# Performance work log

Measured on AMD Instinct MI355X. Metric: run time of the kernel, lower is better.

## Reference

```python
import jax, jax.numpy as jnp
import numpy as np

D = 128          # kg_emb_dim
H = 8            # mha_n_heads
N = 20000        # sub-graph nodes per modality
NNZ = 500000     # incidence entries per modality
E = 5000         # hyperedges per modality
C = 50           # context entities
NENT = 50000     # n_entity (rec vocab)


def hyperconv(x, theta, bias, nodes, edges, num_edges):
    # PyG-style HypergraphConv: out = D^-1 H B^-1 H^T (X Theta) + b
    xt = x @ theta                                             # [N, D]
    ones = jnp.ones(nodes.shape[0], xt.dtype)
    e_sum = jax.ops.segment_sum(xt[nodes], edges, num_segments=num_edges)   # [E, D]
    e_deg = jax.ops.segment_sum(ones, edges, num_segments=num_edges)        # [E]
    m = e_sum / jnp.maximum(e_deg, 1.0)[:, None]               # hyperedge means
    n_sum = jax.ops.segment_sum(m[edges], nodes, num_segments=x.shape[0])   # [N, D]
    n_deg = jax.ops.segment_sum(ones, nodes, num_segments=x.shape[0])       # [N]
    return n_sum / jnp.maximum(n_deg, 1.0)[:, None] + bias


def mha(q_x, kv_x, Wq, bq, Wk, bk, Wv, bv, Wo, bo):
    # torch.nn.MultiheadAttention math, batch of 1 (squeezed)
    dh = D // H
    q = (q_x @ Wq + bq).reshape(-1, H, dh)
    k = (kv_x @ Wk + bk).reshape(-1, H, dh)
    v = (kv_x @ Wv + bv).reshape(-1, H, dh)
    scores = jnp.einsum('qhd,khd->hqk', q, k) / jnp.sqrt(jnp.asarray(dh, q.dtype))
    attn = jax.nn.softmax(scores, axis=-1)
    out = jnp.einsum('hqk,khd->qhd', attn, v).reshape(-1, D)
    return out @ Wo + bo


def self_attn(h, a, b):
    # SelfAttentionBatch: softmax(tanh(h a) b) weighted sum over rows
    e = (jnp.tanh(h @ a) @ b)[:, 0]
    return jax.nn.softmax(e) @ h


def setup_inputs() -> dict:
    ks = jax.random.split(jax.random.key(0), 32)
    s = D ** (-0.5)
    inp = {
        'item_emb':   jax.random.normal(ks[0], (N, D), jnp.float32) * s,
        'entity_emb': jax.random.normal(ks[1], (N, D), jnp.float32) * s,
        'word_emb':   jax.random.normal(ks[2], (N, D), jnp.float32) * s,
        'context_entity': jax.random.normal(ks[3], (C, D), jnp.float32) * s,
        'theta_item':   jax.random.normal(ks[4], (D, D), jnp.float32) * s,
        'bias_item':    jax.random.normal(ks[5], (D,), jnp.float32) * 0.02,
        'theta_entity': jax.random.normal(ks[6], (D, D), jnp.float32) * s,
        'bias_entity':  jax.random.normal(ks[7], (D,), jnp.float32) * 0.02,
        'theta_word':   jax.random.normal(ks[8], (D, D), jnp.float32) * s,
        'bias_word':    jax.random.normal(ks[9], (D,), jnp.float32) * 0.02,
        'Wq': jax.random.normal(ks[10], (D, D), jnp.float32) * s,
        'bq': jax.random.normal(ks[11], (D,), jnp.float32) * 0.02,
        'Wk': jax.random.normal(ks[12], (D, D), jnp.float32) * s,
        'bk': jax.random.normal(ks[13], (D,), jnp.float32) * 0.02,
        'Wv': jax.random.normal(ks[14], (D, D), jnp.float32) * s,
        'bv': jax.random.normal(ks[15], (D,), jnp.float32) * 0.02,
        'Wo': jax.random.normal(ks[16], (D, D), jnp.float32) * s,
        'bo': jax.random.normal(ks[17], (D,), jnp.float32) * 0.02,
        'a_his': jax.random.normal(ks[18], (D, D), jnp.float32) * s,
        'b_his': jax.random.normal(ks[19], (D, 1), jnp.float32) * s,
        'a_kg':  jax.random.normal(ks[20], (D, D), jnp.float32) * s,
        'b_kg':  jax.random.normal(ks[21], (D, 1), jnp.float32) * s,
        'rec_W': jax.random.normal(ks[22], (D, NENT), jnp.float32) * s,
        'rec_b': jax.random.normal(ks[23], (NENT,), jnp.float32) * 0.02,
        'item_nodes':   jax.random.randint(ks[24], (NNZ,), 0, N, jnp.int32),
        'item_edges':   jax.random.randint(ks[25], (NNZ,), 0, E, jnp.int32),
        'entity_nodes': jax.random.randint(ks[26], (NNZ,), 0, N, jnp.int32),
        'entity_edges': jax.random.randint(ks[27], (NNZ,), 0, E, jnp.int32),
        'word_nodes':   jax.random.randint(ks[28], (NNZ,), 0, N, jnp.int32),
        'word_edges':   jax.random.randint(ks[29], (NNZ,), 0, E, jnp.int32),
    }
    return inp


def reference(item_emb, entity_emb, word_emb, context_entity,
              theta_item, bias_item, theta_entity, bias_entity, theta_word, bias_word,
              Wq, bq, Wk, bk, Wv, bv, Wo, bo,
              a_his, b_his, a_kg, b_kg, rec_W, rec_b,
              item_nodes, item_edges, entity_nodes, entity_edges, word_nodes, word_edges):
    ih = hyperconv(item_emb, theta_item, bias_item, item_nodes, item_edges, E)
    eh = hyperconv(entity_emb, theta_entity, bias_entity, entity_nodes, entity_edges, E)
    wh = hyperconv(word_emb, theta_word, bias_word, word_nodes, word_edges, E)
    related = jnp.concatenate([ih, eh, wh], axis=0)            # [3N, D]
    # MHItemAttention: context queries attend over related embeddings
    attentive = mha(context_entity, related, Wq, bq, Wk, bk, Wv, bv, Wo, bo)  # [C, D]
    u = self_attn(attentive, a_his, b_his)                     # [D]
    user = jnp.concatenate([context_entity, u[None]], axis=0)  # [C+1, D]
    user_repr = self_attn(user, a_kg, b_kg)                    # [D]
    scores = user_repr @ rec_W + rec_b                         # [NENT]
    return scores
```

## Files before the change

kernel.cpp:

```cpp
#include <hip/hip_runtime.h>
#include <hip/hip_bf16.h>

#define D_ 128
#define H_ 8
#define N_ 20000
#define NNZ_ 500000
#define E_ 5000
#define C_ 50
#define NENT_ 50000
#define NK_ (3*N_)
#define CAPE_ 192
#define CAPN_ 64
#define ENT_PB 4096
#define NBKT 157
#define BCAP 3648
#define ABLK 123
#define NCH3 118
#define KVBLK 235

struct Ptr3f { const float* p[3]; };
struct Ptr3i { const int* p[3]; };
struct GemmB { const float* A[3]; const float* W[3]; unsigned short* C[3]; };

typedef short bf16x8 __attribute__((ext_vector_type(8)));
typedef float f32x4  __attribute__((ext_vector_type(4)));
typedef float f32x2  __attribute__((ext_vector_type(2)));

__device__ __forceinline__ unsigned short f2b(float f){
  unsigned u = __float_as_uint(f);
  u += 0x7FFFu + ((u>>16)&1u);
  return (unsigned short)(u>>16);
}
__device__ __forceinline__ unsigned pk2(float a, float b){
  return (unsigned)f2b(a) | ((unsigned)f2b(b) << 16);
}
__device__ __forceinline__ float blo(unsigned u){ return __uint_as_float(u<<16); }
__device__ __forceinline__ float bhi(unsigned u){ return __uint_as_float(u & 0xFFFF0000u); }

#define GBATCH(SRC, SREG, LBASE) { \
  uint4 uu[8]; \
  _Pragma("unroll") \
  for (int kk=0;kk<8;kk++){ \
    int idx = __shfl(SREG, (LBASE) + 4*kk + rgrp); \
    uu[kk] = *(const uint4*)((SRC) + (size_t)idx*128 + dl*8); \
  } \
  _Pragma("unroll") \
  for (int kk=0;kk<8;kk++){ \
    a01 += (f32x2){blo(uu[kk].x), bhi(uu[kk].x)}; \
    a23 += (f32x2){blo(uu[kk].y), bhi(uu[kk].y)}; \
    a45 += (f32x2){blo(uu[kk].z), bhi(uu[kk].z)}; \
    a67 += (f32x2){blo(uu[kk].w), bhi(uu[kk].w)}; \
  } }

#define PB_PACK 7500
#define PB_Z    7628
#define PB_Q    7629
#define PB_CTX  7693
#define PB_TOT  7743
__global__ __launch_bounds__(256) void prep(Ptr3f xs, unsigned short* __restrict__ xb,
    const float* __restrict__ Wk, const float* __restrict__ Wv, unsigned short* __restrict__ bfB,
    int* __restrict__ gcnt_e, int* __restrict__ gcnt_n, unsigned short* __restrict__ mzero,
    const float* __restrict__ ctx, const float* __restrict__ Wq, const float* __restrict__ bq,
    unsigned short* __restrict__ bfQ,
    const float* __restrict__ a2, const float* __restrict__ b2, float* __restrict__ e2)
{
  int bid = blockIdx.x, t = threadIdx.x;
  if (bid < PB_PACK){
    int mod = bid / 2500, blk = bid - mod*2500;
    int i4 = blk*256 + t;
    float4 v = *(const float4*)(xs.p[mod] + (size_t)i4*4);
    ushort4 o; o.x=f2b(v.x); o.y=f2b(v.y); o.z=f2b(v.z); o.w=f2b(v.w);
    *(ushort4*)(xb + (size_t)mod*N_*D_ + (size_t)i4*4) = o;
  } else if (bid < PB_Z){
    int idx = (bid - PB_PACK)*256 + t;
    int j  = idx & 7;
    int L  = (idx >> 3) & 63;
    int kb = (idx >> 9) & 3;
    int tt = idx >> 11;
    int k = kb*32 + (L>>4)*8 + j;
    int x = L & 15;
    float v = (tt < 8) ? Wk[(size_t)k*128 + tt*16 + x] : Wv[(size_t)k*128 + (tt-8)*16 + x];
    bfB[idx] = f2b(v);
  } else if (bid == PB_Z){
    for (int i=t; i<3*NBKT; i+=256){ gcnt_e[i]=0; gcnt_n[i]=0; }
    if (t < 64)       ((unsigned*)(xb    + (size_t)60000*128))[t]    = 0u;
    else if (t < 128) ((unsigned*)(mzero + (size_t)15000*128))[t-64] = 0u;
  } else if (bid < PB_CTX){
    int idx = (bid - PB_Q)*256 + t;
    int j  = idx & 7;
    int L  = (idx >> 3) & 63;
    int qt = (idx >> 9) & 3;
    int h  = idx >> 11;
    int k  = ((L>>4)&3)*8 + j;
    int q  = qt*16 + (L & 15);
    float val = 0.f;
    if (k < 16 && q < C_){
      const float* cr = ctx + (size_t)q*128;
      const float* wc = Wq + h*16 + k;
      float s0=0.f,s1=0.f,s2=0.f,s3=0.f;
      for (int d=0; d<128; d+=4){
        s0 = fmaf(cr[d],   wc[(size_t) d   *128], s0);
        s1 = fmaf(cr[d+1], wc[(size_t)(d+1)*128], s1);
        s2 = fmaf(cr[d+2], wc[(size_t)(d+2)*128], s2);
        s3 = fmaf(cr[d+3], wc[(size_t)(d+3)*128], s3);
      }
      val = 0.25f * (s0+s1+s2+s3 + bq[h*16+k]);
    }
    bfQ[idx] = f2b(val);
  } else {
    __shared__ float row[128];
    __shared__ float ps[128][2];
    __shared__ float red[2];
    int q = bid - PB_CTX;
    if (t < 128) row[t] = ctx[(size_t)q*128 + t];
    __syncthreads();
    int c = t & 127, half = t >> 7;
    float s = 0.f;
    int d0 = half*64;
    for (int d=d0; d<d0+64; d+=4){
      s = fmaf(row[d],   a2[(size_t) d   *128 + c], s);
      s = fmaf(row[d+1], a2[(size_t)(d+1)*128 + c], s);
      s = fmaf(row[d+2], a2[(size_t)(d+2)*128 + c], s);
      s = fmaf(row[d+3], a2[(size_t)(d+3)*128 + c], s);
    }
    ps[c][half] = s;
    __syncthreads();
    if (t < 128){
      float v = tanhf(ps[t][0] + ps[t][1]) * b2[t];
      #pragma unroll
      for (int k=32; k>=1; k>>=1) v += __shfl_xor(v, k);
      if ((t & 63) == 0) red[t>>6] = v;
    }
    __syncthreads();
    if (t == 0) e2[q] = red[0] + red[1];
  }
}

__global__ __launch_bounds__(256) void binA(Ptr3i nodes, Ptr3i edges,
    unsigned* __restrict__ pe_part, unsigned* __restrict__ pn_part,
    int* __restrict__ gcnt_e, int* __restrict__ gcnt_n)
{
  __shared__ unsigned lbin[ENT_PB];
  __shared__ int cnt[256], off[256];
  __shared__ int gbase[NBKT];
  __shared__ int wsum[4];
  const int mod = blockIdx.y;
  const int* nd = nodes.p[mod];
  const int* ed = edges.p[mod];
  const int base = blockIdx.x * ENT_PB;
  const int t = threadIdx.x;
  const int lane = t & 63, w = t >> 6;

  int myn[16], mye[16], pos[16];
  #pragma unroll
  for (int k=0;k<16;k++){
    int i = base + t + k*256;
    if (i < NNZ_){ myn[k]=nd[i]; mye[k]=ed[i]; }
    else { myn[k]=-1; mye[k]=-1; }
  }

  cnt[t] = 0;
  __syncthreads();
  #pragma unroll
  for (int k=0;k<16;k++)
    if (mye[k] >= 0) pos[k] = atomicAdd(&cnt[mye[k]>>5], 1);
  __syncthreads();
  {
    int v = cnt[t], s = v;
    #pragma unroll
    for (int d=1; d<64; d<<=1){ int u=__shfl_up(s,d); if (lane>=d) s+=u; }
    if (lane==63) wsum[w]=s;
    __syncthreads();
    int wb=0;
    for (int i=0;i<w;i++) wb+=wsum[i];
    off[t] = wb + s - v;
    __syncthreads();
  }
  #pragma unroll
  for (int k=0;k<16;k++)
    if (mye[k] >= 0)
      lbin[off[mye[k]>>5] + pos[k]] = ((unsigned)mye[k] << 15) | (unsigned)myn[k];
  if (t < NBKT && cnt[t] > 0) gbase[t] = atomicAdd(&gcnt_e[mod*NBKT + t], cnt[t]);
  __syncthreads();
  {
    int total = off[255];
    unsigned* dstreg = pe_part + (size_t)mod*NBKT*BCAP;
    for (int i=t; i<total; i+=256){
      unsigned pk = lbin[i];
      int b = pk >> 20;
      int gp = gbase[b] + (i - off[b]);
      if (gp < BCAP) dstreg[(size_t)b*BCAP + gp] = pk;
    }
  }
  __syncthreads();

  cnt[t] = 0;
  __syncthreads();
  #pragma unroll
  for (int k=0;k<16;k++)
    if (myn[k] >= 0) pos[k] = atomicAdd(&cnt[myn[k]>>7], 1);
  __syncthreads();
  {
    int v = cnt[t], s = v;
    #pragma unroll
    for (int d=1; d<64; d<<=1){ int u=__shfl_up(s,d); if (lane>=d) s+=u; }
    if (lane==63) wsum[w]=s;
    __syncthreads();
    int wb=0;
    for (int i=0;i<w;i++) wb+=wsum[i];
    off[t] = wb + s - v;
    __syncthreads();
  }
  #pragma unroll
  for (int k=0;k<16;k++)
    if (myn[k] >= 0)
      lbin[off[myn[k]>>7] + pos[k]] = ((unsigned)myn[k] << 13) | (unsigned)mye[k];
  if (t < NBKT && cnt[t] > 0) gbase[t] = atomicAdd(&gcnt_n[mod*NBKT + t], cnt[t]);
  __syncthreads();
  {
    int total = off[255];
    unsigned* dstreg = pn_part + (size_t)mod*NBKT*BCAP;
    for (int i=t; i<total; i+=256){
      unsigned pk = lbin[i];
      int b = pk >> 20;
      int gp = gbase[b] + (i - off[b]);
      if (gp < BCAP) dstreg[(size_t)b*BCAP + gp] = pk;
    }
  }
}

__global__ __launch_bounds__(256) void binB(const unsigned* __restrict__ pe_part,
    const unsigned* __restrict__ pn_part,
    const int* __restrict__ gcnt_e, const int* __restrict__ gcnt_n,
    int* __restrict__ cnt_all,
    unsigned short* __restrict__ e_slot, unsigned short* __restrict__ n_slot)
{
  __shared__ unsigned short ls[128*CAPN_];
  __shared__ int lc[128];
  const int y = blockIdx.y, b = blockIdx.x, t = threadIdx.x;
  if (y < 3){
    const int mod = y;
    {
      unsigned short dmy = (unsigned short)(60000 - mod*20000);
      unsigned dd = (unsigned)dmy * 0x10001u;
      unsigned* lsu32 = (unsigned*)ls;
      for (int i=t; i<32*CAPE_/2; i+=256) lsu32[i] = dd;
    }
    if (t < 32) lc[t] = 0;
    __syncthreads();
    int cnt = gcnt_e[mod*NBKT + b];
    if (cnt > BCAP) cnt = BCAP;
    const unsigned* src = pe_part + ((size_t)mod*NBKT + b)*BCAP;
    for (int i=t; i<cnt; i+=256){
      unsigned pk = src[i];
      int el = (pk >> 15) - b*32;
      int n  = pk & 0x7FFF;
      int p = atomicAdd(&lc[el], 1);
      if (p < CAPE_) ls[el*CAPE_ + p] = (unsigned short)n;
    }
    __syncthreads();
    int rows = E_ - b*32; if (rows > 32) rows = 32;
    if (t < rows) cnt_all[mod*(E_+N_) + b*32 + t] = lc[t];
    const unsigned* lsu = (const unsigned*)ls;
    unsigned* dst = (unsigned*)(e_slot + ((size_t)mod*E_ + b*32)*CAPE_);
    int tot = rows*CAPE_/2;
    for (int i=t; i<tot; i+=256) dst[i] = lsu[i];
  } else {
    const int mod = y - 3;
    {
      unsigned short dmy = (unsigned short)(15000 - mod*5000);
      unsigned dd = (unsigned)dmy * 0x10001u;
      unsigned* lsu32 = (unsigned*)ls;
      for (int i=t; i<128*CAPN_/2; i+=256) lsu32[i] = dd;
    }
    if (t < 128) lc[t] = 0;
    __syncthreads();
    int cnt = gcnt_n[mod*NBKT + b];
    if (cnt > BCAP) cnt = BCAP;
    const unsigned* src = pn_part + ((size_t)mod*NBKT + b)*BCAP;
    for (int i=t; i<cnt; i+=256){
      unsigned pk = src[i];
      int nl = (pk >> 13) - b*128;
      int e  = pk & 0x1FFF;
      int p = atomicAdd(&lc[nl], 1);
      if (p < CAPN_) ls[nl*CAPN_ + p] = (unsigned short)e;
    }
    __syncthreads();
    int rows = N_ - b*128; if (rows > 128) rows = 128;
    if (t < rows) cnt_all[mod*(E_+N_) + E_ + b*128 + t] = lc[t];
    const unsigned* lsu = (const unsigned*)ls;
    unsigned* dst = (unsigned*)(n_slot + ((size_t)mod*N_ + b*128)*CAPN_);
    int tot = rows*CAPN_/2;
    for (int i=t; i<tot; i+=256) dst[i] = lsu[i];
  }
}

#define EGB 3752
__global__ __launch_bounds__(256) void e_gather_w(const unsigned short* __restrict__ xb,
    const int* __restrict__ cnt_all, const unsigned short* __restrict__ e_slot,
    float* __restrict__ m_mean)
{
  const int bid = blockIdx.x;
  const int x = bid & 7, k = bid >> 3;
  int mod, r;
  if (x < 6){
    mod = x / 3;
    int li = x - mod*3;
    int c = 417 - (li == 2);
    if (k < c){
      r = k*3 + li;
    } else {
      int hg = 52*x + (x >= 3) + (k - c);
      mod = 2; r = 938 + hg;
      if (r >= E_/4) return;
    }
  } else {
    mod = 2; r = k*2 + (x - 6);
  }
  const int w = threadIdx.x >> 6, lane = threadIdx.x & 63;
  const int rgrp = lane >> 4, dl = lane & 15;
  const int e = r*4 + w;
  const unsigned short* xt = xb + (size_t)mod*N_*D_;
  int cnt = cnt_all[mod*(E_+N_) + e];
  int c2 = (cnt < CAPE_) ? cnt : CAPE_;
  int c2p = (c2 + 31) & ~31;
  const unsigned short* slot = e_slot + ((size_t)mod*E_ + e)*CAPE_;
  int sv0 = slot[lane], sv1 = slot[64 + lane], sv2 = slot[128 + lane];
  f32x2 a01={0.f,0.f}, a23={0.f,0.f}, a45={0.f,0.f}, a67={0.f,0.f};

  if (c2p > 0)   GBATCH(xt, sv0, 0);
  if (c2p > 32)  GBATCH(xt, sv0, 32);
  if (c2p > 64)  GBATCH(xt, sv1, 0);
  if (c2p > 96)  GBATCH(xt, sv1, 32);
  if (c2p > 128) GBATCH(xt, sv2, 0);
  if (c2p > 160) GBATCH(xt, sv2, 32);

  float a0=a01.x, a1=a01.y, a2=a23.x, a3=a23.y, a4=a45.x, a5=a45.y, a6=a67.x, a7=a67.y;
  #pragma unroll
  for (int s=16; s<=32; s<<=1){
    a0 += __shfl_xor(a0, s); a1 += __shfl_xor(a1, s);
    a2 += __shfl_xor(a2, s); a3 += __shfl_xor(a3, s);
    a4 += __shfl_xor(a4, s); a5 += __shfl_xor(a5, s);
    a6 += __shfl_xor(a6, s); a7 += __shfl_xor(a7, s);
  }
  if (rgrp == 0){
    float inv = 1.f / fmaxf((float)cnt, 1.f);
    float* dst = m_mean + ((size_t)mod*E_ + e)*128 + dl*8;
    float4 o1; o1.x=a0*inv; o1.y=a1*inv; o1.z=a2*inv; o1.w=a3*inv;
    float4 o2; o2.x=a4*inv; o2.y=a5*inv; o2.z=a6*inv; o2.w=a7*inv;
    *(float4*)dst = o1;
    *(float4*)(dst + 4) = o2;
  }
}

__global__ __launch_bounds__(256) void gemm_b(GemmB g, int M)
{
  const float* A = g.A[blockIdx.y];
  const float* W = g.W[blockIdx.y];
  unsigned short* Cout = g.C[blockIdx.y];
  __shared__ float As[64][33];
  __shared__ float Ws[32][128];
  const int t  = threadIdx.x;
  const int br = blockIdx.x * 64;
  const int r0 = (t >> 5) * 8;
  const int c0 = (t & 31) * 4;
  const int lr = t >> 2;
  const int lk = (t & 3) * 8;
  const int wk = t >> 5;

  float acc[8][4];
  #pragma unroll
  for (int i=0;i<8;i++){ acc[i][0]=0.f; acc[i][1]=0.f; acc[i][2]=0.f; acc[i][3]=0.f; }

  for (int kb=0; kb<128; kb+=32){
    float av[8];
    const int grow = br + lr;
    if (grow < M){
      const float* p = A + (size_t)grow*128 + kb + lk;
      float4 a = ((const float4*)p)[0], b = ((const float4*)p)[1];
      av[0]=a.x;av[1]=a.y;av[2]=a.z;av[3]=a.w;av[4]=b.x;av[5]=b.y;av[6]=b.z;av[7]=b.w;
    } else {
      #pragma unroll
      for (int j=0;j<8;j++) av[j]=0.f;
    }
    float4 wv4[4];
    #pragma unroll
    for (int kk=0;kk<4;kk++) wv4[kk] = *(const float4*)&W[(size_t)(kb + wk + kk*8)*128 + c0];

    __syncthreads();
    #pragma unroll
    for (int j=0;j<8;j++) As[lr][lk+j] = av[j];
    #pragma unroll
    for (int kk=0;kk<4;kk++) *(float4*)&Ws[wk + kk*8][c0] = wv4[kk];
    __syncthreads();

    #pragma unroll
    for (int k=0;k<32;k++){
      float4 wv = *(const float4*)&Ws[k][c0];
      #pragma unroll
      for (int i=0;i<8;i++){
        float a = As[r0+i][k];
        acc[i][0] = fmaf(a, wv.x, acc[i][0]);
        acc[i][1] = fmaf(a, wv.y, acc[i][1]);
        acc[i][2] = fmaf(a, wv.z, acc[i][2]);
        acc[i][3] = fmaf(a, wv.w, acc[i][3]);
      }
    }
  }

  #pragma unroll
  for (int i=0;i<8;i++){
    int gr = br + r0 + i;
    if (gr < M){
      ushort4 o;
      o.x=f2b(acc[i][0]); o.y=f2b(acc[i][1]); o.z=f2b(acc[i][2]); o.w=f2b(acc[i][3]);
      *(ushort4*)(Cout + (size_t)gr*128 + c0) = o;
    }
  }
}

__global__ __launch_bounds__(256) void n_gather_w(const unsigned short* __restrict__ m_buf,
    const int* __restrict__ cnt_all, const unsigned short* __restrict__ n_slot,
    Ptr3f biases, unsigned short* __restrict__ relbf)
{
  int mod = blockIdx.y;
  int w = threadIdx.x >> 6, lane = threadIdx.x & 63;
  int rgrp = lane >> 4, dl = lane & 15;
  int n = blockIdx.x*4 + w;
  const unsigned short* m = m_buf + (size_t)mod*E_*D_;
  int cnt = cnt_all[mod*(E_+N_) + E_ + n];
  int c2 = (cnt < CAPN_) ? cnt : CAPN_;
  int c2p = (c2 + 31) & ~31;
  const unsigned short* slot = n_slot + ((size_t)mod*N_ + n)*CAPN_;
  int sv = slot[lane];
  f32x2 a01={0.f,0.f}, a23={0.f,0.f}, a45={0.f,0.f}, a67={0.f,0.f};
  if (c2p > 0)  GBATCH(m, sv, 0);
  if (c2p > 32) GBATCH(m, sv, 32);

  float a0=a01.x, a1=a01.y, a2=a23.x, a3=a23.y, a4=a45.x, a5=a45.y, a6=a67.x, a7=a67.y;
  #pragma unroll
  for (int s=16; s<=32; s<<=1){
    a0 += __shfl_xor(a0, s); a1 += __shfl_xor(a1, s);
    a2 += __shfl_xor(a2, s); a3 += __shfl_xor(a3, s);
    a4 += __shfl_xor(a4, s); a5 += __shfl_xor(a5, s);
    a6 += __shfl_xor(a6, s); a7 += __shfl_xor(a7, s);
  }
  if (rgrp == 0){
    float inv = 1.f / fmaxf((float)cnt, 1.f);
    const float* bs = biases.p[mod] + dl*8;
    uint4 o;
    o.x = pk2(a0*inv + bs[0], a1*inv + bs[1]);
    o.y = pk2(a2*inv + bs[2], a3*inv + bs[3]);
    o.z = pk2(a4*inv + bs[4], a5*inv + bs[5]);
    o.w = pk2(a6*inv + bs[6], a7*inv + bs[7]);
    *(uint4*)(relbf + ((size_t)mod*N_ + n)*128 + dl*8) = o;
  }
}

__global__ __launch_bounds__(256) void gemm_kv_mfma(const unsigned short* __restrict__ relbf,
    const unsigned short* __restrict__ bfB, const float* __restrict__ bk,
    const float* __restrict__ bv, unsigned short* __restrict__ Kb,
    unsigned short* __restrict__ Vtg)
{
  __shared__ unsigned short Bs[32768];
  const int t = threadIdx.x, w = t >> 6, L = t & 63;
  const int m = L & 15, quad = L >> 4, x = m;

  {
    const uint4* src = (const uint4*)bfB;
    uint4* dst = (uint4*)Bs;
    for (int i = t; i < 4096; i += 256) dst[i] = src[i];
  }
  __syncthreads();

  const int rowbase = blockIdx.x*256;
  for (int g = 0; g < 4; g++){
    const int j0 = rowbase + g*64 + w*16;

    bf16x8 a[4];
    {
      int row = j0 + m;
      int rowc = (row < NK_) ? row : (NK_-1);
      #pragma unroll
      for (int kb=0; kb<4; kb++)
        a[kb] = *(const bf16x8*)(relbf + (size_t)rowc*128 + kb*32 + quad*8);
    }

    f32x4 acc[16];
    #pragma unroll
    for (int tt=0; tt<16; tt++) acc[tt] = (f32x4){0.f,0.f,0.f,0.f};

    #pragma unroll
    for (int kb=0; kb<4; kb++){
      #pragma unroll
      for (int tt=0; tt<16; tt++){
        bf16x8 b = *(const bf16x8*)&Bs[(((tt*4 + kb)*64 + L) << 3)];
        acc[tt] = __builtin_amdgcn_mfma_f32_16x16x32_bf16(a[kb], b, acc[tt], 0, 0, 0);
      }
    }

    #pragma unroll
    for (int tt=0; tt<16; tt++){
      int h = tt & 7, kv = tt >> 3;
      float bias = (kv ? bv : bk)[h*16 + x];
      #pragma unroll
      for (int r=0; r<4; r++){
        int jr = j0 + quad*4 + r;
        if (jr < NK_){
          unsigned short val = f2b(acc[tt][r] + bias);
          if (kv == 0) Kb[(((size_t)h*NK_ + jr) << 4) + x] = val;
          else         Vtg[((size_t)(h*16 + x))*NK_ + jr] = val;
        }
      }
    }
  }
}

__global__ __launch_bounds__(256) void flash3(const unsigned short* __restrict__ Kb,
    const unsigned short* __restrict__ Vtg, const unsigned short* __restrict__ bfQ,
    float* __restrict__ part)
{
  __shared__ unsigned short P_lds[4][64][40];
  __shared__ float mbuf[4][64][18];
  const int c = blockIdx.x, h = blockIdx.y;
  const int t = threadIdx.x, w = t >> 6, L = t & 63;
  const int n = L & 15, quad = L >> 4;

  bf16x8 qb[4];
  #pragma unroll
  for (int qt=0; qt<4; qt++)
    qb[qt] = *(const bf16x8*)(bfQ + (((h*4 + qt)*64 + L) << 3));

  float Mc[4], Lc[4];
  f32x4 accq[4];
  #pragma unroll
  for (int qt=0; qt<4; qt++){ Mc[qt] = -INFINITY; Lc[qt] = 0.f; accq[qt] = (f32x4){0.f,0.f,0.f,0.f}; }

  const int base = c*512 + w*128;
  unsigned* Pw = (unsigned*)&P_lds[w][0][0];

  for (int tile=0; tile<4; tile++){
    const int j0 = base + tile*32;
    const bool dead = (j0 >= NK_);

    bf16x8 a0 = (bf16x8){0,0,0,0,0,0,0,0};
    bf16x8 a1 = a0;
    if (quad < 2){
      int k0 = j0 + n;      if (k0 > NK_-1) k0 = NK_-1;
      int k1 = j0 + 16 + n; if (k1 > NK_-1) k1 = NK_-1;
      a0 = *(const bf16x8*)(Kb + (((size_t)h*NK_ + k0) << 4) + quad*8);
      a1 = *(const bf16x8*)(Kb + (((size_t)h*NK_ + k1) << 4) + quad*8);
    }
    f32x4 s0[4], s1[4];
    #pragma unroll
    for (int qt=0; qt<4; qt++){
      s0[qt] = __builtin_amdgcn_mfma_f32_16x16x32_bf16(a0, qb[qt], (f32x4){0.f,0.f,0.f,0.f}, 0,0,0);
      s1[qt] = __builtin_amdgcn_mfma_f32_16x16x32_bf16(a1, qb[qt], (f32x4){0.f,0.f,0.f,0.f}, 0,0,0);
    }

    #pragma unroll
    for (int qt=0; qt<4; qt++){
      float mt = s0[qt][0];
      mt = fmaxf(mt, s0[qt][1]); mt = fmaxf(mt, s0[qt][2]); mt = fmaxf(mt, s0[qt][3]);
      mt = fmaxf(mt, s1[qt][0]); mt = fmaxf(mt, s1[qt][1]);
      mt = fmaxf(mt, s1[qt][2]); mt = fmaxf(mt, s1[qt][3]);
      mt = fmaxf(mt, __shfl_xor(mt, 16));
      mt = fmaxf(mt, __shfl_xor(mt, 32));
      float Mn = fmaxf(Mc[qt], mt);
      float corr = __expf(Mc[qt] - Mn);
      Mc[qt] = Mn;
      float p0[4], p1[4];
      #pragma unroll
      for (int r=0;r<4;r++){
        p0[r] = __expf(s0[qt][r] - Mn);
        p1[r] = __expf(s1[qt][r] - Mn);
      }
      if (dead){
        #pragma unroll
        for (int r=0;r<4;r++){ p0[r]=0.f; p1[r]=0.f; }
      }
      float lt = p0[0]+p0[1]+p0[2]+p0[3]+p1[0]+p1[1]+p1[2]+p1[3];
      lt += __shfl_xor(lt, 16);
      lt += __shfl_xor(lt, 32);
      Lc[qt] = Lc[qt]*corr + lt;
      int rb = (qt*16 + n)*20;
      Pw[rb + quad*2]     = pk2(p0[0], p0[1]);
      Pw[rb + quad*2 + 1] = pk2(p0[2], p0[3]);
      Pw[rb + 8 + quad*2]     = pk2(p1[0], p1[1]);
      Pw[rb + 8 + quad*2 + 1] = pk2(p1[2], p1[3]);
      #pragma unroll
      for (int r=0;r<4;r++){
        float cr = __shfl(corr, quad*4 + r);
        accq[qt][r] *= cr;
      }
    }
    __syncthreads();

    bf16x8 bv_;
    {
      int va = j0 + quad*8; if (va > NK_-8) va = NK_-8;
      bv_ = *(const bf16x8*)(Vtg + ((size_t)(h*16 + n))*NK_ + va);
    }
    #pragma unroll
    for (int qt=0; qt<4; qt++){
      bf16x8 pa = *(const bf16x8*)&P_lds[w][qt*16 + n][quad*8];
      accq[qt] = __builtin_amdgcn_mfma_f32_16x16x32_bf16(pa, bv_, accq[qt], 0,0,0);
    }
    __syncthreads();
  }

  #pragma unroll
  for (int qt=0; qt<4; qt++){
    #pragma unroll
    for (int r=0; r<4; r++)
      mbuf[w][qt*16 + quad*4 + r][2 + n] = accq[qt][r];
    if (quad == 0){
      mbuf[w][qt*16 + n][0] = Mc[qt];
      mbuf[w][qt*16 + n][1] = Lc[qt];
    }
  }
  __syncthreads();
  if (t < C_){
    float M = mbuf[0][t][0], Lm = mbuf[0][t][1];
    float A[16];
    #pragma unroll
    for (int i=0;i<16;i++) A[i] = mbuf[0][t][2+i];
    #pragma unroll
    for (int ww=1; ww<4; ww++){
      float pm = mbuf[ww][t][0], pl = mbuf[ww][t][1];
      if (pl > 0.f){
        float mn = fmaxf(M, pm);
        float c1 = __expf(M - mn), c2 = __expf(pm - mn);
        Lm = Lm*c1 + pl*c2;
        #pragma unroll
        for (int i=0;i<16;i++) A[i] = A[i]*c1 + mbuf[ww][t][2+i]*c2;
        M = mn;
      }
    }
    float* pp = part + ((size_t)(h*NCH3 + c)*C_ + t)*18;
    pp[0] = M; pp[1] = Lm;
    #pragma unroll
    for (int i=0;i<16;i++) pp[2+i] = A[i];
  }
}

__global__ __launch_bounds__(512) void merge_oproj_e1(const float* __restrict__ part,
    const float* __restrict__ Wo, const float* __restrict__ bo,
    const float* __restrict__ a1, const float* __restrict__ b1,
    float* __restrict__ attentive, float* __restrict__ e1)
{
  __shared__ float row[128];
  __shared__ float ps[128][4];
  __shared__ float orow[128];
  __shared__ float red[2];
  const int q = blockIdx.x, t = threadIdx.x;
  const int h = t >> 6, lane = t & 63;

  {
    float M = -1e30f, L = 0.f;
    float A[16];
    #pragma unroll
    for (int i=0;i<16;i++) A[i] = 0.f;

    #pragma unroll
    for (int cc=0; cc<2; cc++){
      int c = lane + cc*64;
      if (c < NCH3){
        const float* p = part + ((size_t)(h*NCH3 + c)*C_ + q)*18;
        float pm = p[0], pl = p[1];
        if (pl > 0.f){
          float Mn = fmaxf(M, pm);
          float w1 = __expf(M - Mn), w2 = __expf(pm - Mn);
          L = L*w1 + pl*w2;
          #pragma unroll
          for (int i=0;i<16;i++) A[i] = fmaf(A[i], w1, p[2+i]*w2);
          M = Mn;
        }
      }
    }
    #pragma unroll
    for (int d=32; d>=1; d>>=1){
      float pm = __shfl_xor(M, d);
      float pl = __shfl_xor(L, d);
      float Ao[16];
      #pragma unroll
      for (int i=0;i<16;i++) Ao[i] = __shfl_xor(A[i], d);
      float Mn = fmaxf(M, pm);
      float w1 = __expf(M - Mn), w2 = __expf(pm - Mn);
      L = L*w1 + pl*w2;
      #pragma unroll
      for (int i=0;i<16;i++) A[i] = fmaf(A[i], w1, Ao[i]*w2);
      M = Mn;
    }
    if (lane == 0){
      float invL = 1.f / L;
      #pragma unroll
      for (int i=0;i<16;i++) row[h*16 + i] = A[i]*invL;
    }
  }
  __syncthreads();

  const int c = t & 127, seg = t >> 7;
  {
    float s = 0.f;
    int d0 = seg*32;
    for (int d=d0; d<d0+32; d+=4){
      s = fmaf(row[d],   Wo[(size_t) d   *128 + c], s);
      s = fmaf(row[d+1], Wo[(size_t)(d+1)*128 + c], s);
      s = fmaf(row[d+2], Wo[(size_t)(d+2)*128 + c], s);
      s = fmaf(row[d+3], Wo[(size_t)(d+3)*128 + c], s);
    }
    ps[c][seg] = s;
  }
  __syncthreads();
  if (t < 128){
    float o = ps[t][0]+ps[t][1]+ps[t][2]+ps[t][3] + bo[t];
    attentive[(size_t)q*128 + t] = o;
    orow[t] = o;
  }
  __syncthreads();
  {
    float s = 0.f;
    int d0 = seg*32;
    for (int d=d0; d<d0+32; d+=4){
      s = fmaf(orow[d],   a1[(size_t) d   *128 + c], s);
      s = fmaf(orow[d+1], a1[(size_t)(d+1)*128 + c], s);
      s = fmaf(orow[d+2], a1[(size_t)(d+2)*128 + c], s);
      s = fmaf(orow[d+3], a1[(size_t)(d+3)*128 + c], s);
    }
    ps[c][seg] = s;
  }
  __syncthreads();
  if (t < 128){
    float v = tanhf(ps[t][0]+ps[t][1]+ps[t][2]+ps[t][3]) * b1[t];
    #pragma unroll
    for (int k=32; k>=1; k>>=1) v += __shfl_xor(v, k);
    if ((t & 63) == 0) red[t>>6] = v;
  }
  __syncthreads();
  if (t == 0) e1[q] = red[0] + red[1];
}

__global__ __launch_bounds__(256) void tail_scores(const float* __restrict__ attentive,
    const float* __restrict__ ctx, const float* __restrict__ a2, const float* __restrict__ b2,
    const float* __restrict__ e1, const float* __restrict__ e2,
    const float* __restrict__ recW, const float* __restrict__ recb, float* __restrict__ out)
{
  __shared__ float p[64];
  __shared__ float u[128];
  __shared__ float red[2];
  __shared__ float p2[64];
  __shared__ float ur[128];
  const int t = threadIdx.x;

  if (t == 0){
    float mx=-INFINITY;
    for (int i=0;i<C_;i++) mx=fmaxf(mx,e1[i]);
    float ss=0.f;
    for (int i=0;i<C_;i++){ p[i]=__expf(e1[i]-mx); ss+=p[i]; }
    float inv=1.f/ss;
    for (int i=0;i<C_;i++) p[i]*=inv;
  }
  __syncthreads();
  if (t < 128){
    float s=0.f;
    for (int r=0;r<C_;r++) s = fmaf(p[r], attentive[(size_t)r*128 + t], s);
    u[t] = s;
  }
  __syncthreads();
  if (t < 128){
    float s0=0.f,s1=0.f,s2=0.f,s3=0.f;
    for (int d=0; d<128; d+=4){
      s0 = fmaf(u[d],   a2[(size_t) d   *128 + t], s0);
      s1 = fmaf(u[d+1], a2[(size_t)(d+1)*128 + t], s1);
      s2 = fmaf(u[d+2], a2[(size_t)(d+2)*128 + t], s2);
      s3 = fmaf(u[d+3], a2[(size_t)(d+3)*128 + t], s3);
    }
    float v = tanhf(s0+s1+s2+s3) * b2[t];
    #pragma unroll
    for (int k=32; k>=1; k>>=1) v += __shfl_xor(v, k);
    if ((t & 63) == 0) red[t>>6] = v;
  }
  __syncthreads();
  if (t == 0){
    float elast = red[0] + red[1];
    float mx=elast;
    for (int i=0;i<C_;i++) mx=fmaxf(mx,e2[i]);
    float ss=0.f;
    for (int i=0;i<C_;i++){ p2[i]=__expf(e2[i]-mx); ss+=p2[i]; }
    float pl = __expf(elast-mx); ss += pl;
    float inv=1.f/ss;
    for (int i=0;i<C_;i++) p2[i]*=inv;
    p2[C_] = pl*inv;
  }
  __syncthreads();
  if (t < 128){
    float s=0.f;
    for (int r=0;r<C_;r++) s = fmaf(p2[r], ctx[(size_t)r*128 + t], s);
    s = fmaf(p2[C_], u[t], s);
    ur[t] = s;
  }
  __syncthreads();
  int j = blockIdx.x*256 + t;
  if (j < NENT_){
    float s0=0.f,s1=0.f,s2=0.f,s3=0.f;
    for (int d=0; d<128; d+=4){
      s0 = fmaf(ur[d],   recW[(size_t) d   *NENT_ + j], s0);
      s1 = fmaf(ur[d+1], recW[(size_t)(d+1)*NENT_ + j], s1);
      s2 = fmaf(ur[d+2], recW[(size_t)(d+2)*NENT_ + j], s2);
      s3 = fmaf(ur[d+3], recW[(size_t)(d+3)*NENT_ + j], s3);
    }
    out[j] = s0+s1+s2+s3 + recb[j];
  }
}

extern "C" void kernel_launch(void* const* d_in, const int* in_sizes, int n_in,
                              void* d_out, int out_size, void* d_ws, size_t ws_size,
                              hipStream_t stream)
{
  auto f32 = [&](int i){ return (const float*)d_in[i]; };
  Ptr3i nodes = {{(const int*)d_in[24], (const int*)d_in[26], (const int*)d_in[28]}};
  Ptr3i edges = {{(const int*)d_in[25], (const int*)d_in[27], (const int*)d_in[29]}};

  char* base = (char*)d_ws;
  int*   cnt_all = (int*)base;
  int*   gcnt_e  = (int*)(base + 300064);
  int*   gcnt_n  = gcnt_e + NBKT*3;
  unsigned short* n_slot = (unsigned short*)(base + 300064 + 4096);
  float* m_mean  = (float*)((char*)n_slot + 7680000);
  unsigned short* m_buf = (unsigned short*)((char*)m_mean + 7680000);
  unsigned short* relbf = (unsigned short*)((char*)m_buf + 3840256);
  unsigned short* bfB   = (unsigned short*)((char*)relbf + 15360000);
  unsigned short* bfQ   = (unsigned short*)((char*)bfB + 65536);
  float* attentive = (float*)((char*)bfQ + 32768);
  float* user_repr = (float*)((char*)attentive + 25600);
  float* e1buf     = user_repr + 128;
  float* e2buf     = e1buf + 64;
  float* fpart = (float*)relbf;
  char* U = (char*)(e2buf + 64);
  unsigned* pe_part = (unsigned*)U;
  unsigned* pn_part = pe_part + (size_t)3*NBKT*BCAP;
  unsigned short* e_slot = (unsigned short*)(pn_part + (size_t)3*NBKT*BCAP);
  unsigned short* xb     = e_slot + (size_t)3*E_*CAPE_;
  unsigned short* Kb  = (unsigned short*)U;
  unsigned short* Vtg = Kb + (size_t)H_*NK_*16;

  Ptr3f xs = {{f32(0), f32(1), f32(2)}};
  prep<<<PB_TOT, 256, 0, stream>>>(xs, xb, f32(12), f32(14), bfB, gcnt_e, gcnt_n, m_buf,
                                   f32(3), f32(10), f32(11), bfQ, f32(20), f32(21), e2buf);

  binA<<<dim3(ABLK, 3), 256, 0, stream>>>(nodes, edges, pe_part, pn_part, gcnt_e, gcnt_n);
  binB<<<dim3(NBKT, 6), 256, 0, stream>>>(pe_part, pn_part, gcnt_e, gcnt_n, cnt_all,
                                          e_slot, n_slot);

  e_gather_w<<<EGB, 256, 0, stream>>>(xb, cnt_all, e_slot, m_mean);
  GemmB g;
  for (int mod=0; mod<3; mod++){
    g.A[mod] = m_mean + (size_t)mod*E_*D_;
    g.W[mod] = f32(4 + 2*mod);
    g.C[mod] = m_buf + (size_t)mod*E_*D_;
  }
  gemm_b<<<dim3((E_+63)/64, 3), 256, 0, stream>>>(g, E_);
  Ptr3f biases = {{f32(5), f32(7), f32(9)}};
  n_gather_w<<<dim3(N_/4, 3), 256, 0, stream>>>(m_buf, cnt_all, n_slot, biases, relbf);

  gemm_kv_mfma<<<KVBLK, 256, 0, stream>>>(relbf, bfB, f32(13), f32(15), Kb, Vtg);
  flash3<<<dim3(NCH3, H_), 256, 0, stream>>>(Kb, Vtg, bfQ, fpart);
  merge_oproj_e1<<<C_, 512, 0, stream>>>(fpart, f32(16), f32(17), f32(18), f32(19),
                                         attentive, e1buf);

  tail_scores<<<(NENT_+255)/256, 256, 0, stream>>>(attentive, f32(3), f32(20), f32(21),
                                                   e1buf, e2buf, f32(22), f32(23), (float*)d_out);
}
```

Before: 336.2 us.

## Fuse binning kernels into prep and edge-gather launches to overlap independent work

Moves the first binning pass into the prep kernel as extra blocks, and splits the second binning pass so the node-side binning runs in the same launch as the hyperedge gather. Counter zeroing moves to a memset before the launch. The aim is to overlap independent stages and cut launch and tail idle time. The risk is that the fused kernels carry the larger shared-memory footprint for every block, which may reduce occupancy for the lightweight prep blocks.

```diff
diff --git a/kernel.cpp b/kernel.cpp
--- a/kernel.cpp
+++ b/kernel.cpp
@@ -17,6 +17,9 @@
 #define ABLK 123
 #define NCH3 118
 #define KVBLK 235
+#define BINA_B (3*ABLK)
+#define NBB (3*NBKT)
+#define EGB 3752
 
 struct Ptr3f { const float* p[3]; };
 struct Ptr3i { const int* p[3]; };
@@ -57,14 +60,109 @@
 #define PB_Q    7629
 #define PB_CTX  7693
 #define PB_TOT  7743
-__global__ __launch_bounds__(256) void prep(Ptr3f xs, unsigned short* __restrict__ xb,
+__global__ __launch_bounds__(256) void prep_binA(Ptr3f xs, unsigned short* __restrict__ xb,
     const float* __restrict__ Wk, const float* __restrict__ Wv, unsigned short* __restrict__ bfB,
-    int* __restrict__ gcnt_e, int* __restrict__ gcnt_n, unsigned short* __restrict__ mzero,
+    unsigned short* __restrict__ mzero,
     const float* __restrict__ ctx, const float* __restrict__ Wq, const float* __restrict__ bq,
     unsigned short* __restrict__ bfQ,
-    const float* __restrict__ a2, const float* __restrict__ b2, float* __restrict__ e2)
-{
-  int bid = blockIdx.x, t = threadIdx.x;
+    const float* __restrict__ a2, const float* __restrict__ b2, float* __restrict__ e2,
+    Ptr3i nodes, Ptr3i edges,
+    unsigned* __restrict__ pe_part, unsigned* __restrict__ pn_part,
+    int* __restrict__ gcnt_e, int* __restrict__ gcnt_n)
+{
+  const int t = threadIdx.x;
+  if (blockIdx.x < BINA_B){
+    __shared__ unsigned lbin[ENT_PB];
+    __shared__ int cnt[256], off[256];
+    __shared__ int gbase[NBKT];
+    __shared__ int wsum[4];
+    const int mod = blockIdx.x / ABLK;
+    const int xblk = blockIdx.x - mod*ABLK;
+    const int* nd = nodes.p[mod];
+    const int* ed = edges.p[mod];
+    const int base = xblk * ENT_PB;
+    const int lane = t & 63, w = t >> 6;
+
+    int myn[16], mye[16], pos[16];
+    #pragma unroll
+    for (int k=0;k<16;k++){
+      int i = base + t + k*256;
+      if (i < NNZ_){ myn[k]=nd[i]; mye[k]=ed[i]; }
+      else { myn[k]=-1; mye[k]=-1; }
+    }
+
+    cnt[t] = 0;
+    __syncthreads();
+    #pragma unroll
+    for (int k=0;k<16;k++)
+      if (mye[k] >= 0) pos[k] = atomicAdd(&cnt[mye[k]>>5], 1);
+    __syncthreads();
+    {
+      int v = cnt[t], s = v;
+      #pragma unroll
+      for (int d=1; d<64; d<<=1){ int u=__shfl_up(s,d); if (lane>=d) s+=u; }
+      if (lane==63) wsum[w]=s;
+      __syncthreads();
+      int wb=0;
+      for (int i=0;i<w;i++) wb+=wsum[i];
+      off[t] = wb + s - v;
+      __syncthreads();
+    }
+    #pragma unroll
+    for (int k=0;k<16;k++)
+      if (mye[k] >= 0)
+        lbin[off[mye[k]>>5] + pos[k]] = ((unsigned)mye[k] << 15) | (unsigned)myn[k];
+    if (t < NBKT && cnt[t] > 0) gbase[t] = atomicAdd(&gcnt_e[mod*NBKT + t], cnt[t]);
+    __syncthreads();
+    {
+      int total = off[255];
+      unsigned* dstreg = pe_part + (size_t)mod*NBKT*BCAP;
+      for (int i=t; i<total; i+=256){
+        unsigned pk = lbin[i];
+        int b = pk >> 20;
+        int gp = gbase[b] + (i - off[b]);
+        if (gp < BCAP) dstreg[(size_t)b*BCAP + gp] = pk;
+      }
+    }
+    __syncthreads();
+
+    cnt[t] = 0;
+    __syncthreads();
+    #pragma unroll
+    for (int k=0;k<16;k++)
+      if (myn[k] >= 0) pos[k] = atomicAdd(&cnt[myn[k]>>7], 1);
+    __syncthreads();
+    {
+      int v = cnt[t], s = v;
+      #pragma unroll
+      for (int d=1; d<64; d<<=1){ int u=__shfl_up(s,d); if (lane>=d) s+=u; }
+      if (lane==63) wsum[w]=s;
+      __syncthreads();
+      int wb=0;
+      for (int i=0;i<w;i++) wb+=wsum[i];
+      off[t] = wb + s - v;
+      __syncthreads();
+    }
+    #pragma unroll
+    for (int k=0;k<16;k++)
+      if (myn[k] >= 0)
+        lbin[off[myn[k]>>7] + pos[k]] = ((unsigned)myn[k] << 13) | (unsigned)mye[k];
+    if (t < NBKT && cnt[t] > 0) gbase[t] = atomicAdd(&gcnt_n[mod*NBKT + t], cnt[t]);
+    __syncthreads();
+    {
+      int total = off[255];
+      unsigned* dstreg = pn_part + (size_t)mod*NBKT*BCAP;
+      for (int i=t; i<total; i+=256){
+        unsigned pk = lbin[i];
+        int b = pk >> 20;
+        int gp = gbase[b] + (i - off[b]);
+        if (gp < BCAP) dstreg[(size_t)b*BCAP + gp] = pk;
+      }
+    }
+    return;
+  }
+
+  int bid = blockIdx.x - BINA_B;
   if (bid < PB_PACK){
     int mod = bid / 2500, blk = bid - mod*2500;
     int i4 = blk*256 + t;
@@ -82,7 +180,6 @@
     float v = (tt < 8) ? Wk[(size_t)k*128 + tt*16 + x] : Wv[(size_t)k*128 + (tt-8)*16 + x];
     bfB[idx] = f2b(v);
   } else if (bid == PB_Z){
-    for (int i=t; i<3*NBKT; i+=256){ gcnt_e[i]=0; gcnt_n[i]=0; }
     if (t < 64)       ((unsigned*)(xb    + (size_t)60000*128))[t]    = 0u;
     else if (t < 128) ((unsigned*)(mzero + (size_t)15000*128))[t-64] = 0u;
   } else if (bid < PB_CTX){
@@ -136,137 +233,51 @@
   }
 }
 
-__global__ __launch_bounds__(256) void binA(Ptr3i nodes, Ptr3i edges,
-    unsigned* __restrict__ pe_part, unsigned* __restrict__ pn_part,
-    int* __restrict__ gcnt_e, int* __restrict__ gcnt_n)
-{
-  __shared__ unsigned lbin[ENT_PB];
-  __shared__ int cnt[256], off[256];
-  __shared__ int gbase[NBKT];
-  __shared__ int wsum[4];
-  const int mod = blockIdx.y;
-  const int* nd = nodes.p[mod];
-  const int* ed = edges.p[mod];
-  const int base = blockIdx.x * ENT_PB;
-  const int t = threadIdx.x;
-  const int lane = t & 63, w = t >> 6;
-
-  int myn[16], mye[16], pos[16];
-  #pragma unroll
-  for (int k=0;k<16;k++){
-    int i = base + t + k*256;
-    if (i < NNZ_){ myn[k]=nd[i]; mye[k]=ed[i]; }
-    else { myn[k]=-1; mye[k]=-1; }
-  }
-
-  cnt[t] = 0;
-  __syncthreads();
-  #pragma unroll
-  for (int k=0;k<16;k++)
-    if (mye[k] >= 0) pos[k] = atomicAdd(&cnt[mye[k]>>5], 1);
-  __syncthreads();
+__global__ __launch_bounds__(256) void binB_e(const unsigned* __restrict__ pe_part,
+    const int* __restrict__ gcnt_e, int* __restrict__ cnt_all,
+    unsigned short* __restrict__ e_slot)
+{
+  __shared__ unsigned short ls[32*CAPE_];
+  __shared__ int lc[32];
+  const int mod = blockIdx.y, b = blockIdx.x, t = threadIdx.x;
   {
-    int v = cnt[t], s = v;
-    #pragma unroll
-    for (int d=1; d<64; d<<=1){ int u=__shfl_up(s,d); if (lane>=d) s+=u; }
-    if (lane==63) wsum[w]=s;
-    __syncthreads();
-    int wb=0;
-    for (int i=0;i<w;i++) wb+=wsum[i];
-    off[t] = wb + s - v;
-    __syncthreads();
-  }
-  #pragma unroll
-  for (int k=0;k<16;k++)
-    if (mye[k] >= 0)
-      lbin[off[mye[k]>>5] + pos[k]] = ((unsigned)mye[k] << 15) | (unsigned)myn[k];
-  if (t < NBKT && cnt[t] > 0) gbase[t] = atomicAdd(&gcnt_e[mod*NBKT + t], cnt[t]);
-  __syncthreads();
-  {
-    int total = off[255];
-    unsigned* dstreg = pe_part + (size_t)mod*NBKT*BCAP;
-    for (int i=t; i<total; i+=256){
-      unsigned pk = lbin[i];
-      int b = pk >> 20;
-      int gp = gbase[b] + (i - off[b]);
-      if (gp < BCAP) dstreg[(size_t)b*BCAP + gp] = pk;
-    }
-  }
-  __syncthreads();
-
-  cnt[t] = 0;
-  __syncthreads();
-  #pragma unroll
-  for (int k=0;k<16;k++)
-    if (myn[k] >= 0) pos[k] = atomicAdd(&cnt[myn[k]>>7], 1);
-  __syncthreads();
-  {
-    int v = cnt[t], s = v;
-    #pragma unroll
-    for (int d=1; d<64; d<<=1){ int u=__shfl_up(s,d); if (lane>=d) s+=u; }
-    if (lane==63) wsum[w]=s;
-    __syncthreads();
-    int wb=0;
-    for (int i=0;i<w;i++) wb+=wsum[i];
-    off[t] = wb + s - v;
-    __syncthreads();
-  }
-  #pragma unroll
-  for (int k=0;k<16;k++)
-    if (myn[k] >= 0)
-      lbin[off[myn[k]>>7] + pos[k]] = ((unsigned)myn[k] << 13) | (unsigned)mye[k];
-  if (t < NBKT && cnt[t] > 0) gbase[t] = atomicAdd(&gcnt_n[mod*NBKT + t], cnt[t]);
-  __syncthreads();
-  {
-    int total = off[255];
-    unsigned* dstreg = pn_part + (size_t)mod*NBKT*BCAP;
-    for (int i=t; i<total; i+=256){
-      unsigned pk = lbin[i];
-      int b = pk >> 20;
-      int gp = gbase[b] + (i - off[b]);
-      if (gp < BCAP) dstreg[(size_t)b*BCAP + gp] = pk;
-    }
-  }
-}
-
-__global__ __launch_bounds__(256) void binB(const unsigned* __restrict__ pe_part,
-    const unsigned* __restrict__ pn_part,
-    const int* __restrict__ gcnt_e, const int* __restrict__ gcnt_n,
-    int* __restrict__ cnt_all,
-    unsigned short* __restrict__ e_slot, unsigned short* __restrict__ n_slot)
+    unsigned short dmy = (unsigned short)(60000 - mod*20000);
+    unsigned dd = (unsigned)dmy * 0x10001u;
+    unsigned* lsu32 = (unsigned*)ls;
+    for (int i=t; i<32*CAPE_/2; i+=256) lsu32[i] = dd;
+  }
+  if (t < 32) lc[t] = 0;
+  __syncthreads();
+  int cnt = gcnt_e[mod*NBKT + b];
+  if (cnt > BCAP) cnt = BCAP;
+  const unsigned* src = pe_part + ((size_t)mod*NBKT + b)*BCAP;
+  for (int i=t; i<cnt; i+=256){
+    unsigned pk = src[i];
+    int el = (pk >> 15) - b*32;
+    int n  = pk & 0x7FFF;
+    int p = atomicAdd(&lc[el], 1);
+    if (p < CAPE_) ls[el*CAPE_ + p] = (unsigned short)n;
+  }
+  __syncthreads();
+  int rows = E_ - b*32; if (rows > 32) rows = 32;
+  if (t < rows) cnt_all[mod*(E_+N_) + b*32 + t] = lc[t];
+  const unsigned* lsu = (const unsigned*)ls;
+  unsigned* dst = (unsigned*)(e_slot + ((size_t)mod*E_ + b*32)*CAPE_);
+  int tot = rows*CAPE_/2;
+  for (int i=t; i<tot; i+=256) dst[i] = lsu[i];
+}
+
+__global__ __launch_bounds__(256) void egather_binbn(const unsigned short* __restrict__ xb,
+    const int* __restrict__ cnt_all, const unsigned short* __restrict__ e_slot,
+    float* __restrict__ m_mean,
+    const unsigned* __restrict__ pn_part, const int* __restrict__ gcnt_n,
+    int* __restrict__ cnt_all_w, unsigned short* __restrict__ n_slot)
 {
   __shared__ unsigned short ls[128*CAPN_];
   __shared__ int lc[128];
-  const int y = blockIdx.y, b = blockIdx.x, t = threadIdx.x;
-  if (y < 3){
-    const int mod = y;
-    {
-      unsigned short dmy = (unsigned short)(60000 - mod*20000);
-      unsigned dd = (unsigned)dmy * 0x10001u;
-      unsigned* lsu32 = (unsigned*)ls;
-      for (int i=t; i<32*CAPE_/2; i+=256) lsu32[i] = dd;
-    }
-    if (t < 32) lc[t] = 0;
-    __syncthreads();
-    int cnt = gcnt_e[mod*NBKT + b];
-    if (cnt > BCAP) cnt = BCAP;
-    const unsigned* src = pe_part + ((size_t)mod*NBKT + b)*BCAP;
-    for (int i=t; i<cnt; i+=256){
-      unsigned pk = src[i];
-      int el = (pk >> 15) - b*32;
-      int n  = pk & 0x7FFF;
-      int p = atomicAdd(&lc[el], 1);
-      if (p < CAPE_) ls[el*CAPE_ + p] = (unsigned short)n;
-    }
-    __syncthreads();
-    int rows = E_ - b*32; if (rows > 32) rows = 32;
-    if (t < rows) cnt_all[mod*(E_+N_) + b*32 + t] = lc[t];
-    const unsigned* lsu = (const unsigned*)ls;
-    unsigned* dst = (unsigned*)(e_slot + ((size_t)mod*E_ + b*32)*CAPE_);
-    int tot = rows*CAPE_/2;
-    for (int i=t; i<tot; i+=256) dst[i] = lsu[i];
-  } else {
-    const int mod = y - 3;
+  const int t = threadIdx.x;
+  if (blockIdx.x < NBB){
+    const int mod = blockIdx.x / NBKT, b = blockIdx.x - mod*NBKT;
     {
       unsigned short dmy = (unsigned short)(15000 - mod*5000);
       unsigned dd = (unsigned)dmy * 0x10001u;
@@ -287,21 +298,16 @@
     }
     __syncthreads();
     int rows = N_ - b*128; if (rows > 128) rows = 128;
-    if (t < rows) cnt_all[mod*(E_+N_) + E_ + b*128 + t] = lc[t];
+    if (t < rows) cnt_all_w[mod*(E_+N_) + E_ + b*128 + t] = lc[t];
     const unsigned* lsu = (const unsigned*)ls;
     unsigned* dst = (unsigned*)(n_slot + ((size_t)mod*N_ + b*128)*CAPN_);
     int tot = rows*CAPN_/2;
     for (int i=t; i<tot; i+=256) dst[i] = lsu[i];
-  }
-}
-
-#define EGB 3752
-__global__ __launch_bounds__(256) void e_gather_w(const unsigned short* __restrict__ xb,
-    const int* __restrict__ cnt_all, const unsigned short* __restrict__ e_slot,
-    float* __restrict__ m_mean)
-{
-  const int bid = blockIdx.x;
-  const int x = bid & 7, k = bid >> 3;
+    return;
+  }
+
+  const int bb = blockIdx.x - NBB;
+  const int x = bb & 7, k = bb >> 3;
   int mod, r;
   if (x < 6){
     mod = x / 3;
@@ -317,7 +323,7 @@
   } else {
     mod = 2; r = k*2 + (x - 6);
   }
-  const int w = threadIdx.x >> 6, lane = threadIdx.x & 63;
+  const int w = t >> 6, lane = t & 63;
   const int rgrp = lane >> 4, dl = lane & 15;
   const int e = r*4 + w;
   const unsigned short* xt = xb + (size_t)mod*N_*D_;
@@ -845,15 +851,18 @@
   unsigned short* Kb  = (unsigned short*)U;
   unsigned short* Vtg = Kb + (size_t)H_*NK_*16;
 
+  hipMemsetAsync(gcnt_e, 0, 4096, stream);
+
   Ptr3f xs = {{f32(0), f32(1), f32(2)}};
-  prep<<<PB_TOT, 256, 0, stream>>>(xs, xb, f32(12), f32(14), bfB, gcnt_e, gcnt_n, m_buf,
-                                   f32(3), f32(10), f32(11), bfQ, f32(20), f32(21), e2buf);
-
-  binA<<<dim3(ABLK, 3), 256, 0, stream>>>(nodes, edges, pe_part, pn_part, gcnt_e, gcnt_n);
-  binB<<<dim3(NBKT, 6), 256, 0, stream>>>(pe_part, pn_part, gcnt_e, gcnt_n, cnt_all,
-                                          e_slot, n_slot);
-
-  e_gather_w<<<EGB, 256, 0, stream>>>(xb, cnt_all, e_slot, m_mean);
+  prep_binA<<<BINA_B + PB_TOT, 256, 0, stream>>>(xs, xb, f32(12), f32(14), bfB, m_buf,
+                                   f32(3), f32(10), f32(11), bfQ, f32(20), f32(21), e2buf,
+                                   nodes, edges, pe_part, pn_part, gcnt_e, gcnt_n);
+
+  binB_e<<<dim3(NBKT, 3), 256, 0, stream>>>(pe_part, gcnt_e, cnt_all, e_slot);
+
+  egather_binbn<<<NBB + EGB, 256, 0, stream>>>(xb, cnt_all, e_slot, m_mean,
+                                               pn_part, gcnt_n, cnt_all, n_slot);
+
   GemmB g;
   for (int mod=0; mod<3; mod++){
     g.A[mod] = m_mean + (size_t)mod*E_*D_;
```

New measurement: 334.0 us. Within noise of the previous version (-0.6%).
